# Optimization experiments

Measured on AMD Instinct MI355X. Metric: run time of the kernel, lower is better.

## Reference

```python
import jax, jax.numpy as jnp
import numpy as np

H = 128          # hidden_channels
N_USER = 100000
N_ITEM = 50000
E = 1000000      # number of labeled edges


def setup_inputs() -> dict:
    key = jax.random.key(0)
    ks = jax.random.split(key, 6)
    z_user = jax.random.normal(ks[0], (N_USER, H), dtype=jnp.float32)
    z_item = jax.random.normal(ks[1], (N_ITEM, H), dtype=jnp.float32)
    row = jax.random.randint(ks[2], (E,), 0, N_USER, dtype=jnp.int64 if jax.config.jax_enable_x64 else jnp.int32)
    col = jax.random.randint(ks[3], (E,), 0, N_ITEM, dtype=jnp.int64 if jax.config.jax_enable_x64 else jnp.int32)
    W1 = jax.random.normal(ks[4], (2 * H, H), dtype=jnp.float32) / np.sqrt(2 * H)
    b1 = jnp.zeros((H,), dtype=jnp.float32)
    W2 = jax.random.normal(ks[5], (H, 1), dtype=jnp.float32) / np.sqrt(H)
    b2 = jnp.zeros((1,), dtype=jnp.float32)
    return {"z_user": z_user, "z_item": z_item, "row": row, "col": col,
            "W1": W1, "b1": b1, "W2": W2, "b2": b2}


def reference(z_user, z_item, row, col, W1, b1, W2, b2):
    # z = cat([z_user[row], z_item[col]], -1); lin1(z).relu(); lin2 -> view(-1)
    # Split W1 so we never materialize the [E, 2H] concat explicitly as one buffer:
    # cat([a, b]) @ W1 == a @ W1[:H] + b @ W1[H:]
    W1u, W1i = W1[:H], W1[H:]
    h = z_user[row] @ W1u + z_item[col] @ W1i + b1          # [E, H]
    h = jax.nn.relu(h)
    out = h @ W2 + b2                                        # [E, 1]
    return out.reshape(-1)
```

## Files before the change

### kernel.cpp

```cpp
#include <hip/hip_runtime.h>

#define HH 128

typedef __attribute__((ext_vector_type(8))) short bf16x8;
typedef __attribute__((ext_vector_type(4))) float f32x4;

__device__ inline unsigned short f2bf(float f) {
    unsigned u = __builtin_bit_cast(unsigned, f);
    u += 0x7FFF + ((u >> 16) & 1);
    return (unsigned short)(u >> 16);
}
__device__ inline float bf2f(unsigned short h) {
    return __builtin_bit_cast(float, (unsigned)h << 16);
}

__global__ __launch_bounds__(256) void project_mfma_kernel(
    const float* __restrict__ Z, const float* __restrict__ W,
    const float* __restrict__ bias, int addBias,
    unsigned short* __restrict__ P, int nrows)
{
    __shared__ unsigned short sWt[128 * 128];
    __shared__ unsigned short sOut[64 * 136];

    const int t    = threadIdx.x;
    const int wave = t >> 6;
    const int lane = t & 63;
    const int l16  = lane & 15;
    const int lk8  = (lane >> 4) * 8;

    #pragma unroll 4
    for (int i = 0; i < 16; ++i) {
        int idx = t + i * 256;
        int k   = idx >> 5;
        int c4  = (idx & 31) * 4;
        float4 w = *(const float4*)(W + (size_t)k * HH + c4);
        float wv[4] = {w.x, w.y, w.z, w.w};
        #pragma unroll
        for (int j = 0; j < 4; ++j) {
            int c = c4 + j;
            sWt[c * 128 + (((k >> 3) ^ (c & 15)) << 3) + (k & 7)] = f2bf(wv[j]);
        }
    }

    float b1r[8];
    #pragma unroll
    for (int nt = 0; nt < 8; ++nt)
        b1r[nt] = addBias ? bias[nt * 16 + l16] : 0.f;

    __syncthreads();

    const int ntiles = (nrows + 63) >> 6;
    for (int tile = blockIdx.x; tile < ntiles; tile += gridDim.x) {
        const int rbase = tile << 6;

        f32x4 acc[8];
        #pragma unroll
        for (int nt = 0; nt < 8; ++nt) acc[nt] = (f32x4)0.f;

        int m = rbase + wave * 16 + l16;
        if (m > nrows - 1) m = nrows - 1;
        const float* Zrow = Z + (size_t)m * HH;

        #pragma unroll
        for (int kk = 0; kk < 4; ++kk) {
            float4 z0 = *(const float4*)(Zrow + kk * 32 + lk8);
            float4 z1 = *(const float4*)(Zrow + kk * 32 + lk8 + 4);
            bf16x8 a;
            a[0] = (short)f2bf(z0.x); a[1] = (short)f2bf(z0.y);
            a[2] = (short)f2bf(z0.z); a[3] = (short)f2bf(z0.w);
            a[4] = (short)f2bf(z1.x); a[5] = (short)f2bf(z1.y);
            a[6] = (short)f2bf(z1.z); a[7] = (short)f2bf(z1.w);

            const int chunkSw = ((kk * 4 + (lane >> 4)) ^ l16) << 3;
            #pragma unroll
            for (int nt = 0; nt < 8; ++nt) {
                int c = nt * 16 + l16;
                bf16x8 b = *(const bf16x8*)(sWt + c * 128 + chunkSw);
                acc[nt] = __builtin_amdgcn_mfma_f32_16x16x32_bf16(a, b, acc[nt], 0, 0, 0);
            }
        }

        __syncthreads();
        #pragma unroll
        for (int nt = 0; nt < 8; ++nt) {
            int colc = nt * 16 + l16;
            #pragma unroll
            for (int r = 0; r < 4; ++r) {
                int orow = wave * 16 + (lane >> 4) * 4 + r;
                sOut[orow * 136 + colc] = f2bf(acc[nt][r] + b1r[nt]);
            }
        }
        __syncthreads();
        #pragma unroll
        for (int i = 0; i < 4; ++i) {
            int idx = t + i * 256;
            int r   = idx >> 4;
            int ch  = idx & 15;
            int grow = rbase + r;
            if (grow < nrows)
                *(uint4*)(P + (size_t)grow * HH + ch * 8) =
                    *(const uint4*)(sOut + r * 136 + ch * 8);
        }
    }
}

__global__ __launch_bounds__(256) void edge_bf16_kernel(
    const unsigned short* __restrict__ Pu, const unsigned short* __restrict__ Pi,
    const int* __restrict__ row, const int* __restrict__ col,
    const float* __restrict__ W2, const float* __restrict__ b2,
    float* __restrict__ out, int E)
{
    const int lane16 = threadIdx.x & 15;
    const int gid    = (blockIdx.x * blockDim.x + threadIdx.x) >> 4;
    const int stride = (gridDim.x * blockDim.x) >> 4;
    const int c0     = lane16 * 8;

    float w2r[8];
    #pragma unroll
    for (int j = 0; j < 8; ++j) w2r[j] = W2[c0 + j];
    const float b2s = b2[0];

    for (int e = gid; e < E; e += stride) {
        int u  = row[e];
        int it = col[e];
        uint4 pu = *(const uint4*)(Pu + (size_t)u  * HH + c0);
        uint4 pi = *(const uint4*)(Pi + (size_t)it * HH + c0);
        unsigned puw[4] = {pu.x, pu.y, pu.z, pu.w};
        unsigned piw[4] = {pi.x, pi.y, pi.z, pi.w};
        float p = 0.f;
        #pragma unroll
        for (int q = 0; q < 4; ++q) {
            float a0 = __builtin_bit_cast(float, puw[q] << 16);
            float a1 = __builtin_bit_cast(float, puw[q] & 0xFFFF0000u);
            float c0f = __builtin_bit_cast(float, piw[q] << 16);
            float c1f = __builtin_bit_cast(float, piw[q] & 0xFFFF0000u);
            float h0 = fmaxf(a0 + c0f, 0.f);
            float h1 = fmaxf(a1 + c1f, 0.f);
            p = fmaf(h0, w2r[2 * q],     p);
            p = fmaf(h1, w2r[2 * q + 1], p);
        }
        #pragma unroll
        for (int m = 8; m >= 1; m >>= 1)
            p += __shfl_xor(p, m, 64);
        if (lane16 == 0) out[e] = p + b2s;
    }
}

__global__ __launch_bounds__(256) void edge_direct_kernel(
    const float* __restrict__ zu, const float* __restrict__ zi,
    const int* __restrict__ row, const int* __restrict__ col,
    const float* __restrict__ W1, const float* __restrict__ b1,
    const float* __restrict__ W2, const float* __restrict__ b2,
    float* __restrict__ out, int E)
{
    const int lane   = threadIdx.x & 31;
    const int gid    = (blockIdx.x * blockDim.x + threadIdx.x) >> 5;
    const int stride = (gridDim.x * blockDim.x) >> 5;
    const int c0     = lane * 4;

    const float4 b1v = *(const float4*)(b1 + c0);
    const float4 w2v = *(const float4*)(W2 + c0);
    const float  b2s = b2[0];

    for (int e = gid; e < E; e += stride) {
        int u  = row[e];
        int it = col[e];
        const float* zur = zu + (size_t)u  * HH;
        const float* zir = zi + (size_t)it * HH;
        float4 acc = b1v;
        for (int k = 0; k < HH; ++k) {
            float  zk = zur[k];
            float4 w  = *(const float4*)(W1 + (size_t)k * HH + c0);
            acc.x = fmaf(zk, w.x, acc.x);
            acc.y = fmaf(zk, w.y, acc.y);
            acc.z = fmaf(zk, w.z, acc.z);
            acc.w = fmaf(zk, w.w, acc.w);
        }
        for (int k = 0; k < HH; ++k) {
            float  zk = zir[k];
            float4 w  = *(const float4*)(W1 + (size_t)(HH + k) * HH + c0);
            acc.x = fmaf(zk, w.x, acc.x);
            acc.y = fmaf(zk, w.y, acc.y);
            acc.z = fmaf(zk, w.z, acc.z);
            acc.w = fmaf(zk, w.w, acc.w);
        }
        float p = fmaxf(acc.x, 0.f) * w2v.x;
        p = fmaf(fmaxf(acc.y, 0.f), w2v.y, p);
        p = fmaf(fmaxf(acc.z, 0.f), w2v.z, p);
        p = fmaf(fmaxf(acc.w, 0.f), w2v.w, p);
        #pragma unroll
        for (int m = 16; m >= 1; m >>= 1)
            p += __shfl_xor(p, m, 64);
        if (lane == 0) out[e] = p + b2s;
    }
}

extern "C" void kernel_launch(void* const* d_in, const int* in_sizes, int n_in,
                              void* d_out, int out_size, void* d_ws, size_t ws_size,
                              hipStream_t stream)
{
    const float* z_user = (const float*)d_in[0];
    const float* z_item = (const float*)d_in[1];
    const int*   row    = (const int*)d_in[2];
    const int*   col    = (const int*)d_in[3];
    const float* W1     = (const float*)d_in[4];
    const float* b1     = (const float*)d_in[5];
    const float* W2     = (const float*)d_in[6];
    const float* b2     = (const float*)d_in[7];
    float*       out    = (float*)d_out;

    const int n_user = in_sizes[0] / HH;
    const int n_item = in_sizes[1] / HH;
    const int E      = in_sizes[2];

    const size_t need = ((size_t)n_user + (size_t)n_item) * HH * sizeof(unsigned short);
    if (ws_size >= need) {
        unsigned short* Pu = (unsigned short*)d_ws;
        unsigned short* Pi = Pu + (size_t)n_user * HH;
        project_mfma_kernel<<<768, 256, 0, stream>>>(z_user, W1, b1, 1, Pu, n_user);
        project_mfma_kernel<<<768, 256, 0, stream>>>(z_item, W1 + HH * HH, b1, 0, Pi, n_item);
        edge_bf16_kernel<<<2048, 256, 0, stream>>>(Pu, Pi, row, col, W2, b2, out, E);
    } else {
        edge_direct_kernel<<<2048, 256, 0, stream>>>(z_user, z_item, row, col, W1, b1, W2, b2, out, E);
    }
}
```

Baseline: 112.7 us.

## Merge user/item projections into one launch and unroll edge gather by two

Replaces the two persistent projection launches (768 blocks each) with a single launch. Each block handles exactly two 64-row tiles, taking the user or item half according to its block index, so both projections run concurrently and the second launch disappears. Every block now reloads and bf16-converts the 128x128 weight slice for only two tiles, which adds weight-staging overhead per block. The edge kernel now processes two edges per iteration so more independent gathers are in flight, at the cost of extra registers.

New measurement: 106.1 us. -5.9%, faster.

```diff
diff --git a/kernel.cpp b/kernel.cpp
--- a/kernel.cpp
+++ b/kernel.cpp
@@ -10,17 +10,23 @@
     u += 0x7FFF + ((u >> 16) & 1);
     return (unsigned short)(u >> 16);
 }
-__device__ inline float bf2f(unsigned short h) {
-    return __builtin_bit_cast(float, (unsigned)h << 16);
-}
-
-__global__ __launch_bounds__(256) void project_mfma_kernel(
-    const float* __restrict__ Z, const float* __restrict__ W,
-    const float* __restrict__ bias, int addBias,
-    unsigned short* __restrict__ P, int nrows)
+
+__global__ __launch_bounds__(256) void project_both_kernel(
+    const float* __restrict__ Zu, const float* __restrict__ Zi,
+    const float* __restrict__ W1, const float* __restrict__ b1,
+    unsigned short* __restrict__ Pu, unsigned short* __restrict__ Pi,
+    int n_user, int n_item, int ublocks)
 {
     __shared__ unsigned short sWt[128 * 128];
     __shared__ unsigned short sOut[64 * 136];
+
+    const bool isUser = ((int)blockIdx.x < ublocks);
+    const float* __restrict__ Z = isUser ? Zu : Zi;
+    const float* __restrict__ W = isUser ? W1 : (W1 + HH * HH);
+    unsigned short* __restrict__ P = isUser ? Pu : Pi;
+    const int nrows  = isUser ? n_user : n_item;
+    const int ntiles = (nrows + 63) >> 6;
+    const int tbase  = (isUser ? (int)blockIdx.x : ((int)blockIdx.x - ublocks)) * 2;
 
     const int t    = threadIdx.x;
     const int wave = t >> 6;
@@ -45,12 +51,14 @@
     float b1r[8];
     #pragma unroll
     for (int nt = 0; nt < 8; ++nt)
-        b1r[nt] = addBias ? bias[nt * 16 + l16] : 0.f;
+        b1r[nt] = isUser ? b1[nt * 16 + l16] : 0.f;
 
     __syncthreads();
 
-    const int ntiles = (nrows + 63) >> 6;
-    for (int tile = blockIdx.x; tile < ntiles; tile += gridDim.x) {
+    #pragma unroll 1
+    for (int s = 0; s < 2; ++s) {
+        const int tile = tbase + s;
+        if (tile >= ntiles) break;
         const int rbase = tile << 6;
 
         f32x4 acc[8];
@@ -120,24 +128,59 @@
     for (int j = 0; j < 8; ++j) w2r[j] = W2[c0 + j];
     const float b2s = b2[0];
 
-    for (int e = gid; e < E; e += stride) {
-        int u  = row[e];
-        int it = col[e];
+    int e = gid;
+    for (; e + stride < E; e += 2 * stride) {
+        const int e2 = e + stride;
+        int u0 = row[e],  i0 = col[e];
+        int u1 = row[e2], i1 = col[e2];
+        uint4 pu0 = *(const uint4*)(Pu + (size_t)u0 * HH + c0);
+        uint4 pi0 = *(const uint4*)(Pi + (size_t)i0 * HH + c0);
+        uint4 pu1 = *(const uint4*)(Pu + (size_t)u1 * HH + c0);
+        uint4 pi1 = *(const uint4*)(Pi + (size_t)i1 * HH + c0);
+
+        unsigned a0[4] = {pu0.x, pu0.y, pu0.z, pu0.w};
+        unsigned b0[4] = {pi0.x, pi0.y, pi0.z, pi0.w};
+        unsigned a1[4] = {pu1.x, pu1.y, pu1.z, pu1.w};
+        unsigned b1w[4] = {pi1.x, pi1.y, pi1.z, pi1.w};
+
+        float p0 = 0.f, p1 = 0.f;
+        #pragma unroll
+        for (int q = 0; q < 4; ++q) {
+            float x0 = __builtin_bit_cast(float, a0[q] << 16);
+            float x1 = __builtin_bit_cast(float, a0[q] & 0xFFFF0000u);
+            float y0 = __builtin_bit_cast(float, b0[q] << 16);
+            float y1 = __builtin_bit_cast(float, b0[q] & 0xFFFF0000u);
+            p0 = fmaf(fmaxf(x0 + y0, 0.f), w2r[2 * q],     p0);
+            p0 = fmaf(fmaxf(x1 + y1, 0.f), w2r[2 * q + 1], p0);
+            float u0f = __builtin_bit_cast(float, a1[q] << 16);
+            float u1f = __builtin_bit_cast(float, a1[q] & 0xFFFF0000u);
+            float v0f = __builtin_bit_cast(float, b1w[q] << 16);
+            float v1f = __builtin_bit_cast(float, b1w[q] & 0xFFFF0000u);
+            p1 = fmaf(fmaxf(u0f + v0f, 0.f), w2r[2 * q],     p1);
+            p1 = fmaf(fmaxf(u1f + v1f, 0.f), w2r[2 * q + 1], p1);
+        }
+        #pragma unroll
+        for (int m = 8; m >= 1; m >>= 1) {
+            p0 += __shfl_xor(p0, m, 64);
+            p1 += __shfl_xor(p1, m, 64);
+        }
+        if (lane16 == 0) { out[e] = p0 + b2s; out[e2] = p1 + b2s; }
+    }
+    if (e < E) {
+        int u = row[e], it = col[e];
         uint4 pu = *(const uint4*)(Pu + (size_t)u  * HH + c0);
         uint4 pi = *(const uint4*)(Pi + (size_t)it * HH + c0);
-        unsigned puw[4] = {pu.x, pu.y, pu.z, pu.w};
-        unsigned piw[4] = {pi.x, pi.y, pi.z, pi.w};
+        unsigned a[4] = {pu.x, pu.y, pu.z, pu.w};
+        unsigned b[4] = {pi.x, pi.y, pi.z, pi.w};
         float p = 0.f;
         #pragma unroll
         for (int q = 0; q < 4; ++q) {
-            float a0 = __builtin_bit_cast(float, puw[q] << 16);
-            float a1 = __builtin_bit_cast(float, puw[q] & 0xFFFF0000u);
-            float c0f = __builtin_bit_cast(float, piw[q] << 16);
-            float c1f = __builtin_bit_cast(float, piw[q] & 0xFFFF0000u);
-            float h0 = fmaxf(a0 + c0f, 0.f);
-            float h1 = fmaxf(a1 + c1f, 0.f);
-            p = fmaf(h0, w2r[2 * q],     p);
-            p = fmaf(h1, w2r[2 * q + 1], p);
+            float x0 = __builtin_bit_cast(float, a[q] << 16);
+            float x1 = __builtin_bit_cast(float, a[q] & 0xFFFF0000u);
+            float y0 = __builtin_bit_cast(float, b[q] << 16);
+            float y1 = __builtin_bit_cast(float, b[q] & 0xFFFF0000u);
+            p = fmaf(fmaxf(x0 + y0, 0.f), w2r[2 * q],     p);
+            p = fmaf(fmaxf(x1 + y1, 0.f), w2r[2 * q + 1], p);
         }
         #pragma unroll
         for (int m = 8; m >= 1; m >>= 1)
@@ -217,8 +260,12 @@
     if (ws_size >= need) {
         unsigned short* Pu = (unsigned short*)d_ws;
         unsigned short* Pi = Pu + (size_t)n_user * HH;
-        project_mfma_kernel<<<768, 256, 0, stream>>>(z_user, W1, b1, 1, Pu, n_user);
-        project_mfma_kernel<<<768, 256, 0, stream>>>(z_item, W1 + HH * HH, b1, 0, Pi, n_item);
+        const int utiles  = (n_user + 63) >> 6;
+        const int itiles  = (n_item + 63) >> 6;
+        const int ublocks = (utiles + 1) >> 1;
+        const int iblocks = (itiles + 1) >> 1;
+        project_both_kernel<<<ublocks + iblocks, 256, 0, stream>>>(
+            z_user, z_item, W1, b1, Pu, Pi, n_user, n_item, ublocks);
         edge_bf16_kernel<<<2048, 256, 0, stream>>>(Pu, Pi, row, col, W2, b2, out, E);
     } else {
         edge_direct_kernel<<<2048, 256, 0, stream>>>(z_user, z_item, row, col, W1, b1, W2, b2, out, E);
```
